# Kernel tuning notes

Measured on AMD Instinct MI355X. Metric: run time of the kernel, lower is better.

## Reference

```python
import jax, jax.numpy as jnp
import numpy as np

R_MIN, R_MAX = 0.8, 0.99  # stability ring bounds from the module (used only at init)

def _is_fast_len(n):
    if n <= 2:
        return True
    x = n
    for p in (2, 3, 5):
        while x % p == 0:
            x //= p
    return x == 1

def next_fast_len(n):
    if n <= 2:
        return n
    m = n
    while not _is_fast_len(m):
        m += 1
    return m

def setup_inputs() -> dict:
    key = jax.random.key(0)
    k1, k2, k3 = jax.random.split(key, 3)
    B, L, C, H, W = 2, 24, 32, 128, 256
    R = 32  # lru_rank
    x = jax.random.normal(k1, (B, L, C, H, W), dtype=jnp.float32)
    # params_log_base = stack([nu_log, theta_log]); init exactly as the torch module does
    u1 = jax.random.uniform(k2, (C, R), dtype=jnp.float32)
    u2 = jax.random.uniform(k3, (C, R), dtype=jnp.float32)
    nu_log = jnp.log(-0.5 * jnp.log(u1 * (R_MAX ** 2 - R_MIN ** 2) + R_MIN ** 2))
    theta_log = jnp.log(u2 * (2.0 * np.pi))
    params_log_base = jnp.stack([nu_log, theta_log], axis=0)  # (2, C, R)
    return {"x": x, "params_log_base": params_log_base}

def reference(x, params_log_base):
    # x: (B, L, C, H, W); params_log_base: (2, C, R)
    B, L, C, H, W = x.shape
    nu = jnp.exp(params_log_base[0])       # (C, R) > 0, lambda magnitude = exp(-nu)
    theta = jnp.exp(params_log_base[1])    # (C, R) phase
    lam_mag = jnp.exp(-nu)
    gamma = jnp.sqrt(jnp.maximum(1.0 - lam_mag * lam_mag, 1e-12))  # input normalization
    # Causal LRU impulse response: k[c, t] = sum_r gamma[c,r] * Re(lambda[c,r]^t)
    t = jnp.arange(L, dtype=x.dtype)                     # (L,)
    decay = jnp.exp(-t[:, None, None] * nu[None])        # (L, C, R)
    osc = jnp.cos(t[:, None, None] * theta[None])        # (L, C, R)
    k = jnp.einsum('tcr,cr->ct', decay * osc, gamma)     # (C, L)
    # FFT-based causal global convolution along the sequence axis
    Lf = next_fast_len(2 * L)
    Xf = jnp.fft.rfft(x, n=Lf, axis=1)                   # (B, F, C, H, W) complex
    Kf = jnp.fft.rfft(k, n=Lf, axis=1)                   # (C, F)
    Yf = Xf * jnp.transpose(Kf)[None, :, :, None, None]
    y = jnp.fft.irfft(Yf, n=Lf, axis=1)[:, :L]           # crop back to causal length
    return y.astype(x.dtype)
```

## Files before the change

kernel.cpp:

```cpp
#include <hip/hip_runtime.h>
#include <hip/hip_bf16.h>

constexpr int BB = 2;
constexpr int L  = 24;
constexpr int C  = 32;
constexpr int H  = 128;
constexpr int W  = 256;
constexpr int HW = H * W;
constexpr int R  = 32;


__global__ __launch_bounds__(256) void convlru_kernel(
    const void* __restrict__ xraw,
    const void* __restrict__ praw,
    float* __restrict__ y)
{
    __shared__ float kk_lds[L];

    const int lane = threadIdx.x & 63;
    const unsigned int wx = ((const unsigned int*)xraw)[lane];
    const unsigned int wp = ((const unsigned int*)praw)[lane];
    const unsigned int hbx = (wx >> 8) & 0xFFu;
    const unsigned int hbp = (wp >> 8) & 0xFFu;
    const bool hitx = (hbx >= 0x3Cu && hbx <= 0x40u) || (hbx >= 0xBCu && hbx <= 0xC0u);
    const bool hitp = (hbp == 0xBFu) || (hbp == 0xC0u);
    const bool x_is_bf16 = __popcll(__ballot(hitx)) >= 32;
    const bool p_is_bf16 = __popcll(__ballot(hitp)) >= 32;

    const int plane = blockIdx.y;
    const int c = plane & (C - 1);
    const int b = plane >> 5;

    const size_t ebase = ((size_t)b * L * C + (size_t)c) * HW
                       + (size_t)blockIdx.x * 512 + (size_t)threadIdx.x * 2;

    float x0[L], x1[L];
    if (x_is_bf16) {
        const unsigned short* xs = (const unsigned short*)xraw;
        #pragma unroll
        for (int l = 0; l < L; ++l) {
            unsigned int w = *(const unsigned int*)(xs + ebase + (size_t)l * C * HW);
            x0[l] = __uint_as_float(w << 16);
            x1[l] = __uint_as_float(w & 0xffff0000u);
        }
    } else {
        const float* xf = (const float*)xraw;
        #pragma unroll
        for (int l = 0; l < L; ++l) {
            float2 v = *(const float2*)(xf + ebase + (size_t)l * C * HW);
            x0[l] = v.x;
            x1[l] = v.y;
        }
    }

    if (threadIdx.x < L) {
        const float t = (float)threadIdx.x;
        float acc = 0.f;
        #pragma unroll 8
        for (int r = 0; r < R; ++r) {
            float p0, p1;
            if (p_is_bf16) {
                const __hip_bfloat16* pb = (const __hip_bfloat16*)praw;
                p0 = __bfloat162float(pb[c * R + r]);
                p1 = __bfloat162float(pb[C * R + c * R + r]);
            } else {
                const float* pf = (const float*)praw;
                p0 = pf[c * R + r];
                p1 = pf[C * R + c * R + r];
            }
            float nu    = expf(p0);
            float theta = expf(p1);
            float lam   = expf(-nu);
            float gamma = sqrtf(fmaxf(1.0f - lam * lam, 1e-12f));
            acc = fmaf(gamma * expf(-t * nu), cosf(t * theta), acc);
        }
        kk_lds[threadIdx.x] = acc;
    }
    __syncthreads();

    float kk[L];
    #pragma unroll
    for (int t = 0; t < L; ++t) kk[t] = kk_lds[t];

    #pragma unroll
    for (int l = 0; l < L; ++l) {
        float a0 = 0.f, a1 = 0.f;
        #pragma unroll
        for (int t = 0; t <= l; ++t) {
            a0 = fmaf(kk[t], x0[l - t], a0);
            a1 = fmaf(kk[t], x1[l - t], a1);
        }
        float2 o; o.x = a0; o.y = a1;
        *(float2*)(y + ebase + (size_t)l * C * HW) = o;
    }
}

extern "C" void kernel_launch(void* const* d_in, const int* in_sizes, int n_in,
                              void* d_out, int out_size, void* d_ws, size_t ws_size,
                              hipStream_t stream) {
    const void* x;
    const void* params;
    if (n_in >= 2 && in_sizes[0] == 2 * C * R) { params = d_in[0]; x = d_in[1]; }
    else                                        { x = d_in[0]; params = d_in[1]; }
    float* y = (float*)d_out;

    dim3 grid(HW / 512, BB * C);
    convlru_kernel<<<grid, 256, 0, stream>>>(x, params, y);
}
```

Before: 352.6 us.

## Precompute LRU kernel taps in separate launch and widen main kernel to float4

```diff
diff --git a/kernel.cpp b/kernel.cpp
--- a/kernel.cpp
+++ b/kernel.cpp
@@ -8,102 +8,104 @@
 constexpr int W  = 256;
 constexpr int HW = H * W;
 constexpr int R  = 32;
+constexpr int LSTRIDE = C * HW;
 
 
-__global__ __launch_bounds__(256) void convlru_kernel(
-    const void* __restrict__ xraw,
-    const void* __restrict__ praw,
+__global__ __launch_bounds__(256) void k_precompute(const void* __restrict__ praw,
+                                                    float* __restrict__ kk_out)
+{
+    const int lane = threadIdx.x & 63;
+    const unsigned int wp  = ((const unsigned int*)praw)[lane];
+    const unsigned int hbp = (wp >> 8) & 0xFFu;
+    const bool hitp = (hbp == 0xBFu) || (hbp == 0xC0u);
+    const bool p_is_bf16 = __popcll(__ballot(hitp)) >= 32;
+
+    const int id = blockIdx.x * 256 + threadIdx.x;
+    if (id >= C * L) return;
+    const int c  = id / L;
+    const int ti = id - c * L;
+    const float t = (float)ti;
+
+    float acc = 0.f;
+    #pragma unroll 8
+    for (int r = 0; r < R; ++r) {
+        float p0, p1;
+        if (p_is_bf16) {
+            const __hip_bfloat16* pb = (const __hip_bfloat16*)praw;
+            p0 = __bfloat162float(pb[c * R + r]);
+            p1 = __bfloat162float(pb[C * R + c * R + r]);
+        } else {
+            const float* pf = (const float*)praw;
+            p0 = pf[c * R + r];
+            p1 = pf[C * R + c * R + r];
+        }
+        float nu    = expf(p0);
+        float theta = expf(p1);
+        float lam   = expf(-nu);
+        float gamma = sqrtf(fmaxf(1.0f - lam * lam, 1e-12f));
+        acc = fmaf(gamma * expf(-t * nu), cosf(t * theta), acc);
+    }
+    kk_out[id] = acc;
+}
+
+__global__ __launch_bounds__(256) void convlru_main(
+    const float* __restrict__ x,
+    const float* __restrict__ kk_g,
     float* __restrict__ y)
 {
-    __shared__ float kk_lds[L];
-
-    const int lane = threadIdx.x & 63;
-    const unsigned int wx = ((const unsigned int*)xraw)[lane];
-    const unsigned int wp = ((const unsigned int*)praw)[lane];
-    const unsigned int hbx = (wx >> 8) & 0xFFu;
-    const unsigned int hbp = (wp >> 8) & 0xFFu;
-    const bool hitx = (hbx >= 0x3Cu && hbx <= 0x40u) || (hbx >= 0xBCu && hbx <= 0xC0u);
-    const bool hitp = (hbp == 0xBFu) || (hbp == 0xC0u);
-    const bool x_is_bf16 = __popcll(__ballot(hitx)) >= 32;
-    const bool p_is_bf16 = __popcll(__ballot(hitp)) >= 32;
-
     const int plane = blockIdx.y;
     const int c = plane & (C - 1);
     const int b = plane >> 5;
 
-    const size_t ebase = ((size_t)b * L * C + (size_t)c) * HW
-                       + (size_t)blockIdx.x * 512 + (size_t)threadIdx.x * 2;
-
-    float x0[L], x1[L];
-    if (x_is_bf16) {
-        const unsigned short* xs = (const unsigned short*)xraw;
+    float kk[L];
+    {
+        const float* kc = kk_g + c * L;
         #pragma unroll
-        for (int l = 0; l < L; ++l) {
-            unsigned int w = *(const unsigned int*)(xs + ebase + (size_t)l * C * HW);
-            x0[l] = __uint_as_float(w << 16);
-            x1[l] = __uint_as_float(w & 0xffff0000u);
-        }
-    } else {
-        const float* xf = (const float*)xraw;
-        #pragma unroll
-        for (int l = 0; l < L; ++l) {
-            float2 v = *(const float2*)(xf + ebase + (size_t)l * C * HW);
-            x0[l] = v.x;
-            x1[l] = v.y;
-        }
+        for (int t = 0; t < L; ++t)
+            kk[t] = __uint_as_float(
+                __builtin_amdgcn_readfirstlane(__float_as_uint(kc[t])));
     }
 
-    if (threadIdx.x < L) {
-        const float t = (float)threadIdx.x;
-        float acc = 0.f;
-        #pragma unroll 8
-        for (int r = 0; r < R; ++r) {
-            float p0, p1;
-            if (p_is_bf16) {
-                const __hip_bfloat16* pb = (const __hip_bfloat16*)praw;
-                p0 = __bfloat162float(pb[c * R + r]);
-                p1 = __bfloat162float(pb[C * R + c * R + r]);
-            } else {
-                const float* pf = (const float*)praw;
-                p0 = pf[c * R + r];
-                p1 = pf[C * R + c * R + r];
-            }
-            float nu    = expf(p0);
-            float theta = expf(p1);
-            float lam   = expf(-nu);
-            float gamma = sqrtf(fmaxf(1.0f - lam * lam, 1e-12f));
-            acc = fmaf(gamma * expf(-t * nu), cosf(t * theta), acc);
-        }
-        kk_lds[threadIdx.x] = acc;
-    }
-    __syncthreads();
+    const unsigned int ebase = (unsigned int)(b * L * C + c) * (unsigned int)HW
+                             + blockIdx.x * 1024u + threadIdx.x * 4u;
+    const float* xb = x + ebase;
+    float*       yb = y + ebase;
 
-    float kk[L];
+    float4 xv[L];
     #pragma unroll
-    for (int t = 0; t < L; ++t) kk[t] = kk_lds[t];
+    for (int l = 0; l < L; ++l)
+        xv[l] = *(const float4*)(xb + (unsigned int)l * (unsigned int)LSTRIDE);
+
+    __builtin_amdgcn_sched_barrier(0);
 
     #pragma unroll
     for (int l = 0; l < L; ++l) {
-        float a0 = 0.f, a1 = 0.f;
+        float4 a = make_float4(0.f, 0.f, 0.f, 0.f);
         #pragma unroll
         for (int t = 0; t <= l; ++t) {
-            a0 = fmaf(kk[t], x0[l - t], a0);
-            a1 = fmaf(kk[t], x1[l - t], a1);
+            const float4 xt = xv[l - t];
+            a.x = fmaf(kk[t], xt.x, a.x);
+            a.y = fmaf(kk[t], xt.y, a.y);
+            a.z = fmaf(kk[t], xt.z, a.z);
+            a.w = fmaf(kk[t], xt.w, a.w);
         }
-        float2 o; o.x = a0; o.y = a1;
-        *(float2*)(y + ebase + (size_t)l * C * HW) = o;
+        *(float4*)(yb + (unsigned int)l * (unsigned int)LSTRIDE) = a;
     }
 }
 
 extern "C" void kernel_launch(void* const* d_in, const int* in_sizes, int n_in,
                               void* d_out, int out_size, void* d_ws, size_t ws_size,
-                              hipStream_t stream) {
+                              hipStream_t stream)
+{
     const void* x;
     const void* params;
     if (n_in >= 2 && in_sizes[0] == 2 * C * R) { params = d_in[0]; x = d_in[1]; }
     else                                        { x = d_in[0]; params = d_in[1]; }
-    float* y = (float*)d_out;
 
-    dim3 grid(HW / 512, BB * C);
-    convlru_kernel<<<grid, 256, 0, stream>>>(x, params, y);
+    float* kk = (float*)d_ws;
+
+    k_precompute<<<dim3((C * L + 255) / 256), dim3(256), 0, stream>>>(params, kk);
+
+    dim3 grid(HW / 1024, BB * C);
+    convlru_main<<<grid, dim3(256), 0, stream>>>((const float*)x, kk, (float*)d_out);
 }
```

Result: slower. 363.3 us (+3.0%).
